# Optimization experiments

Hardware: AMD Instinct MI355X
Metric: run time of the kernel (lower is better)

## Reference

```python
import jax, jax.numpy as jnp
import numpy as np

B = 16384
IN = 512
H = 512

def setup_inputs() -> dict:
    key = jax.random.key(0)
    k1, k2, k3, k4, k5, k6 = jax.random.split(key, 6)
    s_in = 1.0 / np.sqrt(IN + H)
    return {
        "x": jax.random.normal(k1, (B, IN), dtype=jnp.float32),
        "h": jax.random.normal(k2, (B, H), dtype=jnp.float32),
        # lin_in: (IN+H) -> 2H ; stored as [in_features, out_features]
        "W_in": jax.random.uniform(k3, (IN + H, 2 * H), minval=-s_in, maxval=s_in, dtype=jnp.float32),
        "b_in": jax.random.uniform(k4, (2 * H,), minval=-s_in, maxval=s_in, dtype=jnp.float32),
        # lin_out: (IN+H) -> H
        "W_out": jax.random.uniform(k5, (IN + H, H), minval=-s_in, maxval=s_in, dtype=jnp.float32),
        "b_out": jax.random.uniform(k6, (H,), minval=-s_in, maxval=s_in, dtype=jnp.float32),
    }

def reference(x, h, W_in, b_in, W_out, b_out):
    xh = jnp.concatenate([x, h], axis=1)              # [B, IN+H]
    lin = xh @ W_in + b_in                             # [B, 2H]
    learn_pre, forget_pre = jnp.split(lin, 2, axis=1)  # each [B, H]
    learn = jnp.tanh(learn_pre)
    forget_mult = jax.nn.sigmoid(forget_pre)
    h_new = forget_mult * h + (1.0 - forget_mult) * learn
    xh2 = jnp.concatenate([x, h_new], axis=1)          # [B, IN+H]
    out = jnp.tanh(xh2 @ W_out + b_out)                # [B, H]
    return (out, h_new)
```

## Files before the change

### kernel.cpp

```cpp
#include <hip/hip_runtime.h>
#include <cstdint>

typedef unsigned short ushort_t;
typedef __attribute__((ext_vector_type(4))) float f32x4;
typedef __attribute__((ext_vector_type(8))) __bf16 bf16x8;
typedef __attribute__((ext_vector_type(8))) unsigned short ushort8;

#define NB 16384
#define DK 1024

__device__ __forceinline__ unsigned short f2b(float f) {
    unsigned u = __builtin_bit_cast(unsigned, f);
    unsigned r = u + 0x7fffu + ((u >> 16) & 1u);
    return (unsigned short)(r >> 16);
}
__device__ __forceinline__ float b2f(ushort_t b) {
    unsigned u = ((unsigned)b) << 16;
    return __builtin_bit_cast(float, u);
}
__device__ __forceinline__ float fast_sigmoid(float x) {
    return __fdividef(1.0f, 1.0f + __expf(-x));
}
__device__ __forceinline__ float fast_tanh(float x) {
    return __fdividef(2.0f, 1.0f + __expf(-2.0f * x)) - 1.0f;
}

__device__ __forceinline__ void gll16(const void* g, void* lds) {
    __builtin_amdgcn_global_load_lds(
        (__attribute__((address_space(1))) unsigned int*)(uintptr_t)g,
        (__attribute__((address_space(3))) unsigned int*)(unsigned int)(uintptr_t)lds,
        16, 0, 0);
}


__global__ __launch_bounds__(256) void k_f32_to_bf16(const float* __restrict__ s,
                                                     ushort_t* __restrict__ d) {
    size_t g = (size_t)blockIdx.x * 256 + threadIdx.x;
    const float* p = s + g * 8;
    f32x4 f0 = *(const f32x4*)p;
    f32x4 f1 = *(const f32x4*)(p + 4);
    ushort8 o;
#pragma unroll
    for (int j = 0; j < 4; ++j) { o[j] = f2b(f0[j]); o[j + 4] = f2b(f1[j]); }
    *(ushort8*)(d + g * 8) = o;
}

__global__ __launch_bounds__(256) void k_transpose_w(const float* __restrict__ W,
                                                     ushort_t* __restrict__ Wt, int ncols) {
    __shared__ float tile[32][33];
    int n0 = blockIdx.x * 32, k0 = blockIdx.y * 32;
    int tx = threadIdx.x, ty = threadIdx.y;
#pragma unroll
    for (int i = 0; i < 32; i += 8)
        tile[ty + i][tx] = W[(size_t)(k0 + ty + i) * ncols + n0 + tx];
    __syncthreads();
#pragma unroll
    for (int i = 0; i < 32; i += 8)
        Wt[(size_t)(n0 + ty + i) * DK + k0 + tx] = f2b(tile[tx][ty + i]);
}

__global__ __launch_bounds__(256, 2) void k_gemm1(
    const ushort_t* __restrict__ XB, const ushort_t* __restrict__ HB,
    const ushort_t* __restrict__ WT, const float* __restrict__ b_in,
    float* __restrict__ hnew, ushort_t* __restrict__ HN) {
    __shared__ ushort_t As[2][128 * 32];
    __shared__ ushort_t BsL[2][128 * 32];
    __shared__ ushort_t BsF[2][128 * 32];

    const int t = threadIdx.x;
    const int lane = t & 63;
    const int wave = t >> 6;
    const int wm = wave >> 1, wn = wave & 1;
    const int m0 = blockIdx.x * 128;
    const int n0 = blockIdx.y * 128;

    f32x4 accL[4][4] = {};
    f32x4 accF[4][4] = {};

    const int srow = t >> 2;
    const int skel = (t & 3) * 8;
    const size_t arow = (size_t)(m0 + srow) * 512;
    const ushort_t* gBL = WT + (size_t)(n0 + srow) * DK + skel;
    const ushort_t* gBF = WT + (size_t)(n0 + 512 + srow) * DK + skel;

    auto stage = [&](int it, int buf) {
        const int kt = it * 32;
        const ushort_t* abase =
            (kt < 512) ? (XB + arow + kt + skel) : (HB + arow + (kt - 512) + skel);
        ushort_t* a = &As[buf][t * 8];
        ushort_t* bl = &BsL[buf][t * 8];
        ushort_t* bf = &BsF[buf][t * 8];
        gll16(abase, a);
        gll16(abase + 64 * 512, a + 64 * 32);
        gll16(gBL + kt, bl);
        gll16(gBL + kt + 64 * DK, bl + 64 * 32);
        gll16(gBF + kt, bf);
        gll16(gBF + kt + 64 * DK, bf + 64 * 32);
    };

    const int fr = lane & 15;
    const int kq = (lane >> 4) * 8;

    stage(0, 0);
    int cur = 0;
    for (int it = 0; it < 32; ++it) {
        asm volatile("s_waitcnt vmcnt(0)" ::: "memory");
        __syncthreads();
        if (it + 1 < 32) stage(it + 1, cur ^ 1);

        bf16x8 av[4], blv[4], bfv[4];
#pragma unroll
        for (int i = 0; i < 4; ++i) {
            av[i]  = *(const bf16x8*)(&As[cur][(wm * 64 + i * 16 + fr) * 32 + kq]);
            blv[i] = *(const bf16x8*)(&BsL[cur][(wn * 64 + i * 16 + fr) * 32 + kq]);
            bfv[i] = *(const bf16x8*)(&BsF[cur][(wn * 64 + i * 16 + fr) * 32 + kq]);
        }
#pragma unroll
        for (int i = 0; i < 4; ++i)
#pragma unroll
            for (int j = 0; j < 4; ++j) {
                accL[i][j] = __builtin_amdgcn_mfma_f32_16x16x32_bf16(av[i], blv[j], accL[i][j], 0, 0, 0);
                accF[i][j] = __builtin_amdgcn_mfma_f32_16x16x32_bf16(av[i], bfv[j], accF[i][j], 0, 0, 0);
            }
        cur ^= 1;
    }

    const int fq = lane >> 4;
    float bl4[4], bf4[4];
#pragma unroll
    for (int j = 0; j < 4; ++j) {
        const int c = n0 + wn * 64 + j * 16 + fr;
        bl4[j] = b_in[c];
        bf4[j] = b_in[c + 512];
    }
#pragma unroll
    for (int i = 0; i < 4; ++i)
#pragma unroll
        for (int j = 0; j < 4; ++j) {
            const int c = n0 + wn * 64 + j * 16 + fr;
#pragma unroll
            for (int r = 0; r < 4; ++r) {
                const int row = m0 + wm * 64 + i * 16 + fq * 4 + r;
                float lp = accL[i][j][r] + bl4[j];
                float fp = accF[i][j][r] + bf4[j];
                float hv = b2f(HB[(size_t)row * 512 + c]);
                float fm = fast_sigmoid(fp);
                float lr = fast_tanh(lp);
                float hn = fm * hv + (1.0f - fm) * lr;
                hnew[(size_t)row * 512 + c] = hn;
                HN[(size_t)row * 512 + c] = f2b(hn);
            }
        }
}

__global__ __launch_bounds__(256, 2) void k_gemm2(
    const ushort_t* __restrict__ XB, const ushort_t* __restrict__ HN,
    const ushort_t* __restrict__ WT, const float* __restrict__ b_out,
    float* __restrict__ out) {
    __shared__ ushort_t As[2][128 * 32];
    __shared__ ushort_t Bs[2][128 * 32];

    const int t = threadIdx.x;
    const int lane = t & 63;
    const int wave = t >> 6;
    const int wm = wave >> 1, wn = wave & 1;
    const int m0 = blockIdx.x * 128;
    const int n0 = blockIdx.y * 128;

    f32x4 acc[4][4] = {};

    const int srow = t >> 2;
    const int skel = (t & 3) * 8;
    const size_t arow = (size_t)(m0 + srow) * 512;
    const ushort_t* gB = WT + (size_t)(n0 + srow) * DK + skel;

    auto stage = [&](int it, int buf) {
        const int kt = it * 32;
        const ushort_t* abase =
            (kt < 512) ? (XB + arow + kt + skel) : (HN + arow + (kt - 512) + skel);
        ushort_t* a = &As[buf][t * 8];
        ushort_t* b = &Bs[buf][t * 8];
        gll16(abase, a);
        gll16(abase + 64 * 512, a + 64 * 32);
        gll16(gB + kt, b);
        gll16(gB + kt + 64 * DK, b + 64 * 32);
    };

    const int fr = lane & 15;
    const int kq = (lane >> 4) * 8;

    stage(0, 0);
    int cur = 0;
    for (int it = 0; it < 32; ++it) {
        asm volatile("s_waitcnt vmcnt(0)" ::: "memory");
        __syncthreads();
        if (it + 1 < 32) stage(it + 1, cur ^ 1);

        bf16x8 av[4], bv[4];
#pragma unroll
        for (int i = 0; i < 4; ++i) {
            av[i] = *(const bf16x8*)(&As[cur][(wm * 64 + i * 16 + fr) * 32 + kq]);
            bv[i] = *(const bf16x8*)(&Bs[cur][(wn * 64 + i * 16 + fr) * 32 + kq]);
        }
#pragma unroll
        for (int i = 0; i < 4; ++i)
#pragma unroll
            for (int j = 0; j < 4; ++j)
                acc[i][j] = __builtin_amdgcn_mfma_f32_16x16x32_bf16(av[i], bv[j], acc[i][j], 0, 0, 0);
        cur ^= 1;
    }

    const int fq = lane >> 4;
#pragma unroll
    for (int i = 0; i < 4; ++i)
#pragma unroll
        for (int j = 0; j < 4; ++j) {
            const int c = n0 + wn * 64 + j * 16 + fr;
#pragma unroll
            for (int r = 0; r < 4; ++r) {
                const int row = m0 + wm * 64 + i * 16 + fq * 4 + r;
                out[(size_t)row * 512 + c] = fast_tanh(acc[i][j][r] + b_out[c]);
            }
        }
}

extern "C" void kernel_launch(void* const* d_in, const int* in_sizes, int n_in,
                              void* d_out, int out_size, void* d_ws, size_t ws_size,
                              hipStream_t stream) {
    const float* x = (const float*)d_in[0];
    const float* h = (const float*)d_in[1];
    const float* W_in = (const float*)d_in[2];
    const float* b_in = (const float*)d_in[3];
    const float* W_out = (const float*)d_in[4];
    const float* b_out = (const float*)d_in[5];

    float* out = (float*)d_out;
    float* hnew = out + (size_t)NB * 512;

    ushort_t* XB = (ushort_t*)d_ws;
    ushort_t* HB = XB + (size_t)NB * 512;
    ushort_t* HN = HB + (size_t)NB * 512;
    ushort_t* WTI = HN + (size_t)NB * 512;
    ushort_t* WTO = WTI + (size_t)1024 * 1024;

    k_f32_to_bf16<<<4096, 256, 0, stream>>>(x, XB);
    k_f32_to_bf16<<<4096, 256, 0, stream>>>(h, HB);
    k_transpose_w<<<dim3(32, 32), dim3(32, 8), 0, stream>>>(W_in, WTI, 1024);
    k_transpose_w<<<dim3(16, 32), dim3(32, 8), 0, stream>>>(W_out, WTO, 512);
    k_gemm1<<<dim3(128, 4), 256, 0, stream>>>(XB, HB, WTI, b_in, hnew, HN);
    k_gemm2<<<dim3(128, 4), 256, 0, stream>>>(XB, HN, WTO, b_out, out);
}
```

Before: 93.75 us.

## Triple-buffer LDS staging in both GEMMs with partial vmcnt waits

Both GEMM kernels move from double to triple buffering. Loads for the tile two iterations ahead are issued while the current tile is computed, and the wait is relaxed to a partial vmcnt so one tile's loads stay in flight. MFMA sections are wrapped in s_setprio, and gemm2's launch bounds request 3 blocks per CU. The goal is to hide global load latency; the cost is more LDS per block, which may reduce occupancy for gemm1, along with register pressure from the raised occupancy target in gemm2.

Result: no change. 94.47 us (+0.8%).

```diff
diff --git a/kernel.cpp b/kernel.cpp
--- a/kernel.cpp
+++ b/kernel.cpp
@@ -63,9 +63,9 @@
     const ushort_t* __restrict__ XB, const ushort_t* __restrict__ HB,
     const ushort_t* __restrict__ WT, const float* __restrict__ b_in,
     float* __restrict__ hnew, ushort_t* __restrict__ HN) {
-    __shared__ ushort_t As[2][128 * 32];
-    __shared__ ushort_t BsL[2][128 * 32];
-    __shared__ ushort_t BsF[2][128 * 32];
+    __shared__ ushort_t As[3][128 * 32];
+    __shared__ ushort_t BsL[3][128 * 32];
+    __shared__ ushort_t BsF[3][128 * 32];
 
     const int t = threadIdx.x;
     const int lane = t & 63;
@@ -87,7 +87,7 @@
         const int kt = it * 32;
         const ushort_t* abase =
             (kt < 512) ? (XB + arow + kt + skel) : (HB + arow + (kt - 512) + skel);
-        ushort_t* a = &As[buf][t * 8];
+        ushort_t* a  = &As[buf][t * 8];
         ushort_t* bl = &BsL[buf][t * 8];
         ushort_t* bf = &BsF[buf][t * 8];
         gll16(abase, a);
@@ -102,11 +102,17 @@
     const int kq = (lane >> 4) * 8;
 
     stage(0, 0);
+    stage(1, 1);
     int cur = 0;
     for (int it = 0; it < 32; ++it) {
-        asm volatile("s_waitcnt vmcnt(0)" ::: "memory");
-        __syncthreads();
-        if (it + 1 < 32) stage(it + 1, cur ^ 1);
+        if (it < 31) asm volatile("s_waitcnt vmcnt(6)" ::: "memory");
+        else         asm volatile("s_waitcnt vmcnt(0)" ::: "memory");
+        __builtin_amdgcn_s_barrier();
+        asm volatile("" ::: "memory");
+        __builtin_amdgcn_sched_barrier(0);
+
+        int wbuf = cur - 1; if (wbuf < 0) wbuf = 2;
+        if (it < 30) stage(it + 2, wbuf);
 
         bf16x8 av[4], blv[4], bfv[4];
 #pragma unroll
@@ -115,6 +121,7 @@
             blv[i] = *(const bf16x8*)(&BsL[cur][(wn * 64 + i * 16 + fr) * 32 + kq]);
             bfv[i] = *(const bf16x8*)(&BsF[cur][(wn * 64 + i * 16 + fr) * 32 + kq]);
         }
+        __builtin_amdgcn_s_setprio(1);
 #pragma unroll
         for (int i = 0; i < 4; ++i)
 #pragma unroll
@@ -122,7 +129,8 @@
                 accL[i][j] = __builtin_amdgcn_mfma_f32_16x16x32_bf16(av[i], blv[j], accL[i][j], 0, 0, 0);
                 accF[i][j] = __builtin_amdgcn_mfma_f32_16x16x32_bf16(av[i], bfv[j], accF[i][j], 0, 0, 0);
             }
-        cur ^= 1;
+        __builtin_amdgcn_s_setprio(0);
+        cur = (cur == 2) ? 0 : cur + 1;
     }
 
     const int fq = lane >> 4;
@@ -153,12 +161,12 @@
         }
 }
 
-__global__ __launch_bounds__(256, 2) void k_gemm2(
+__global__ __launch_bounds__(256, 3) void k_gemm2(
     const ushort_t* __restrict__ XB, const ushort_t* __restrict__ HN,
     const ushort_t* __restrict__ WT, const float* __restrict__ b_out,
     float* __restrict__ out) {
-    __shared__ ushort_t As[2][128 * 32];
-    __shared__ ushort_t Bs[2][128 * 32];
+    __shared__ ushort_t As[3][128 * 32];
+    __shared__ ushort_t Bs[3][128 * 32];
 
     const int t = threadIdx.x;
     const int lane = t & 63;
@@ -190,11 +198,17 @@
     const int kq = (lane >> 4) * 8;
 
     stage(0, 0);
+    stage(1, 1);
     int cur = 0;
     for (int it = 0; it < 32; ++it) {
-        asm volatile("s_waitcnt vmcnt(0)" ::: "memory");
-        __syncthreads();
-        if (it + 1 < 32) stage(it + 1, cur ^ 1);
+        if (it < 31) asm volatile("s_waitcnt vmcnt(4)" ::: "memory");
+        else         asm volatile("s_waitcnt vmcnt(0)" ::: "memory");
+        __builtin_amdgcn_s_barrier();
+        asm volatile("" ::: "memory");
+        __builtin_amdgcn_sched_barrier(0);
+
+        int wbuf = cur - 1; if (wbuf < 0) wbuf = 2;
+        if (it < 30) stage(it + 2, wbuf);
 
         bf16x8 av[4], bv[4];
 #pragma unroll
@@ -202,12 +216,14 @@
             av[i] = *(const bf16x8*)(&As[cur][(wm * 64 + i * 16 + fr) * 32 + kq]);
             bv[i] = *(const bf16x8*)(&Bs[cur][(wn * 64 + i * 16 + fr) * 32 + kq]);
         }
+        __builtin_amdgcn_s_setprio(1);
 #pragma unroll
         for (int i = 0; i < 4; ++i)
 #pragma unroll
             for (int j = 0; j < 4; ++j)
                 acc[i][j] = __builtin_amdgcn_mfma_f32_16x16x32_bf16(av[i], bv[j], acc[i][j], 0, 0, 0);
-        cur ^= 1;
+        __builtin_amdgcn_s_setprio(0);
+        cur = (cur == 2) ? 0 : cur + 1;
     }
 
     const int fq = lane >> 4;
```

## Restructure GEMMs into 256-row, 8-wave tiles with XOR-swizzled LDS and interleaved prefetch

Applied to the files above, without the earlier changes.

Both GEMM kernels move to 512-thread blocks with 256x128 output tiles and K-tiles of 64. Global-to-LDS loads are split into quarter-stages issued between MFMA phases, with partial vmcnt waits, raw barriers and s_setprio. The intent is to overlap memory with compute and cut LDS bank conflicts. The bf16 activation and weight buffers are written pre-swizzled (XOR on the column within each 64-element chunk) so LDS reads avoid conflicts, and the two conversion launches are merged into one. The cost is one block per CU, 128KB of LDS in gemm1, and fragile hand-tuned wait counts.

Result: faster. 86.60 us (-7.6%).

```diff
diff --git a/kernel.cpp b/kernel.cpp
--- a/kernel.cpp
+++ b/kernel.cpp
@@ -8,6 +8,8 @@
 
 #define NB 16384
 #define DK 1024
+
+#define MFMA16(a, b, c) __builtin_amdgcn_mfma_f32_16x16x32_bf16(a, b, c, 0, 0, 0)
 
 __device__ __forceinline__ unsigned short f2b(float f) {
     unsigned u = __builtin_bit_cast(unsigned, f);
@@ -33,16 +35,26 @@
 }
 
 
-__global__ __launch_bounds__(256) void k_f32_to_bf16(const float* __restrict__ s,
-                                                     ushort_t* __restrict__ d) {
-    size_t g = (size_t)blockIdx.x * 256 + threadIdx.x;
+__global__ __launch_bounds__(256) void k_cvt(const float* __restrict__ x,
+                                             const float* __restrict__ h,
+                                             ushort_t* __restrict__ XB,
+                                             ushort_t* __restrict__ HB) {
+    int b = blockIdx.x;
+    const float* s;
+    ushort_t* d;
+    if (b < 4096) { s = x; d = XB; } else { s = h; d = HB; b -= 4096; }
+    size_t g = (size_t)b * 256 + threadIdx.x;
     const float* p = s + g * 8;
     f32x4 f0 = *(const f32x4*)p;
     f32x4 f1 = *(const f32x4*)(p + 4);
     ushort8 o;
 #pragma unroll
     for (int j = 0; j < 4; ++j) { o[j] = f2b(f0[j]); o[j + 4] = f2b(f1[j]); }
-    *(ushort8*)(d + g * 8) = o;
+    size_t fi = g * 8;
+    int row = (int)(fi >> 9);
+    int c = (int)(fi & 511);
+    int swc = (c & ~63) | ((c & 63) ^ ((row & 7) << 3));
+    *(ushort8*)(d + (size_t)row * 512 + swc) = o;
 }
 
 __global__ __launch_bounds__(256) void k_transpose_w(const float* __restrict__ W,
@@ -55,171 +67,233 @@
         tile[ty + i][tx] = W[(size_t)(k0 + ty + i) * ncols + n0 + tx];
     __syncthreads();
 #pragma unroll
-    for (int i = 0; i < 32; i += 8)
-        Wt[(size_t)(n0 + ty + i) * DK + k0 + tx] = f2b(tile[tx][ty + i]);
-}
-
-__global__ __launch_bounds__(256, 2) void k_gemm1(
+    for (int i = 0; i < 32; i += 8) {
+        int n = n0 + ty + i;
+        int k = k0 + tx;
+        int kk = (k & ~63) | ((k & 63) ^ ((n & 7) << 3));
+        Wt[(size_t)n * DK + kk] = f2b(tile[tx][ty + i]);
+    }
+}
+
+__global__ __launch_bounds__(512, 1) void k_gemm1(
     const ushort_t* __restrict__ XB, const ushort_t* __restrict__ HB,
     const ushort_t* __restrict__ WT, const float* __restrict__ b_in,
     float* __restrict__ hnew, ushort_t* __restrict__ HN) {
-    __shared__ ushort_t As[2][128 * 32];
-    __shared__ ushort_t BsL[2][128 * 32];
-    __shared__ ushort_t BsF[2][128 * 32];
+    __shared__ ushort_t As[2][2][128 * 64];
+    __shared__ ushort_t Bs[2][2][128 * 64];
 
     const int t = threadIdx.x;
     const int lane = t & 63;
-    const int wave = t >> 6;
-    const int wm = wave >> 1, wn = wave & 1;
-    const int m0 = blockIdx.x * 128;
+    const int wid = t >> 6;
+    const int wm = wid >> 2, wn = wid & 3;
+    const int m0 = blockIdx.x * 256;
     const int n0 = blockIdx.y * 128;
 
-    f32x4 accL[4][4] = {};
-    f32x4 accF[4][4] = {};
-
-    const int srow = t >> 2;
-    const int skel = (t & 3) * 8;
-    const size_t arow = (size_t)(m0 + srow) * 512;
-    const ushort_t* gBL = WT + (size_t)(n0 + srow) * DK + skel;
-    const ushort_t* gBF = WT + (size_t)(n0 + 512 + srow) * DK + skel;
-
-    auto stage = [&](int it, int buf) {
-        const int kt = it * 32;
-        const ushort_t* abase =
-            (kt < 512) ? (XB + arow + kt + skel) : (HB + arow + (kt - 512) + skel);
-        ushort_t* a = &As[buf][t * 8];
-        ushort_t* bl = &BsL[buf][t * 8];
-        ushort_t* bf = &BsF[buf][t * 8];
-        gll16(abase, a);
-        gll16(abase + 64 * 512, a + 64 * 32);
-        gll16(gBL + kt, bl);
-        gll16(gBL + kt + 64 * DK, bl + 64 * 32);
-        gll16(gBF + kt, bf);
-        gll16(gBF + kt + 64 * DK, bf + 64 * 32);
-    };
-
-    const int fr = lane & 15;
-    const int kq = (lane >> 4) * 8;
-
-    stage(0, 0);
-    int cur = 0;
-    for (int it = 0; it < 32; ++it) {
-        asm volatile("s_waitcnt vmcnt(0)" ::: "memory");
-        __syncthreads();
-        if (it + 1 < 32) stage(it + 1, cur ^ 1);
-
-        bf16x8 av[4], blv[4], bfv[4];
-#pragma unroll
-        for (int i = 0; i < 4; ++i) {
-            av[i]  = *(const bf16x8*)(&As[cur][(wm * 64 + i * 16 + fr) * 32 + kq]);
-            blv[i] = *(const bf16x8*)(&BsL[cur][(wn * 64 + i * 16 + fr) * 32 + kq]);
-            bfv[i] = *(const bf16x8*)(&BsF[cur][(wn * 64 + i * 16 + fr) * 32 + kq]);
-        }
-#pragma unroll
-        for (int i = 0; i < 4; ++i)
-#pragma unroll
-            for (int j = 0; j < 4; ++j) {
-                accL[i][j] = __builtin_amdgcn_mfma_f32_16x16x32_bf16(av[i], blv[j], accL[i][j], 0, 0, 0);
-                accF[i][j] = __builtin_amdgcn_mfma_f32_16x16x32_bf16(av[i], bfv[j], accF[i][j], 0, 0, 0);
-            }
-        cur ^= 1;
+    const int srow = t >> 3;
+    const int schk = (t & 7) * 8;
+
+    const int fr = lane & 15, fq = lane >> 4;
+    const int xr = (lane & 7) << 3;
+
+    f32x4 accL[8][2] = {};
+    f32x4 accF[8][2] = {};
+
+#define G1_STAGE_A(tile, half) do { \
+        int kt_ = (tile) * 64; \
+        const ushort_t* s_ = (kt_ < 512) \
+            ? (XB + (size_t)(m0 + (half) * 128 + srow) * 512 + kt_ + schk) \
+            : (HB + (size_t)(m0 + (half) * 128 + srow) * 512 + (kt_ - 512) + schk); \
+        ushort_t* d_ = &As[(tile) & 1][half][t * 8]; \
+        gll16(s_, d_); \
+        gll16(s_ + 64 * 512, d_ + 64 * 64); \
+    } while (0)
+
+#define G1_STAGE_B(tile, half) do { \
+        int kt_ = (tile) * 64; \
+        const ushort_t* s_ = WT + (size_t)((half) * 512 + n0 + srow) * DK + kt_ + schk; \
+        ushort_t* d_ = &Bs[(tile) & 1][half][t * 8]; \
+        gll16(s_, d_); \
+        gll16(s_ + 64 * DK, d_ + 64 * 64); \
+    } while (0)
+
+#define G1_LDA(cb, r, kk) (*(const bf16x8*)&As[cb][wm][((r) * 16 + fr) * 64 + (((kk) * 32 + fq * 8) ^ xr)])
+#define G1_LDB(cb, half, j, kk) (*(const bf16x8*)&Bs[cb][half][(wn * 32 + (j) * 16 + fr) * 64 + (((kk) * 32 + fq * 8) ^ xr)])
+
+    G1_STAGE_A(0, 0); G1_STAGE_A(0, 1); G1_STAGE_B(0, 0); G1_STAGE_B(0, 1);
+    G1_STAGE_A(1, 0);
+
+    bf16x8 a[8], b0, b1;
+    for (int i = 0; i < 16; ++i) {
+        const int cb = i & 1;
+        if (i < 15) G1_STAGE_A(i + 1, 1);
+        if (i < 15) asm volatile("s_waitcnt vmcnt(4)" ::: "memory");
+        else        asm volatile("s_waitcnt vmcnt(0)" ::: "memory");
+        asm volatile("s_barrier" ::: "memory");
+#pragma unroll
+        for (int r = 0; r < 8; ++r) a[r] = G1_LDA(cb, r, 0);
+        b0 = G1_LDB(cb, 0, 0, 0); b1 = G1_LDB(cb, 0, 1, 0);
+        __builtin_amdgcn_s_setprio(1);
+#pragma unroll
+        for (int r = 0; r < 8; ++r) {
+            accL[r][0] = MFMA16(a[r], b0, accL[r][0]);
+            accL[r][1] = MFMA16(a[r], b1, accL[r][1]);
+        }
+        __builtin_amdgcn_s_setprio(0);
+        asm volatile("s_barrier" ::: "memory");
+        if (i < 15) G1_STAGE_B(i + 1, 0);
+        b0 = G1_LDB(cb, 1, 0, 0); b1 = G1_LDB(cb, 1, 1, 0);
+        __builtin_amdgcn_s_setprio(1);
+#pragma unroll
+        for (int r = 0; r < 8; ++r) {
+            accF[r][0] = MFMA16(a[r], b0, accF[r][0]);
+            accF[r][1] = MFMA16(a[r], b1, accF[r][1]);
+        }
+        __builtin_amdgcn_s_setprio(0);
+        asm volatile("s_barrier" ::: "memory");
+        if (i < 15) G1_STAGE_B(i + 1, 1);
+#pragma unroll
+        for (int r = 0; r < 8; ++r) a[r] = G1_LDA(cb, r, 1);
+        b0 = G1_LDB(cb, 0, 0, 1); b1 = G1_LDB(cb, 0, 1, 1);
+        __builtin_amdgcn_s_setprio(1);
+#pragma unroll
+        for (int r = 0; r < 8; ++r) {
+            accL[r][0] = MFMA16(a[r], b0, accL[r][0]);
+            accL[r][1] = MFMA16(a[r], b1, accL[r][1]);
+        }
+        __builtin_amdgcn_s_setprio(0);
+        asm volatile("s_barrier" ::: "memory");
+        if (i < 14) G1_STAGE_A(i + 2, 0);
+        b0 = G1_LDB(cb, 1, 0, 1); b1 = G1_LDB(cb, 1, 1, 1);
+        __builtin_amdgcn_s_setprio(1);
+#pragma unroll
+        for (int r = 0; r < 8; ++r) {
+            accF[r][0] = MFMA16(a[r], b0, accF[r][0]);
+            accF[r][1] = MFMA16(a[r], b1, accF[r][1]);
+        }
+        __builtin_amdgcn_s_setprio(0);
     }
 
-    const int fq = lane >> 4;
-    float bl4[4], bf4[4];
-#pragma unroll
-    for (int j = 0; j < 4; ++j) {
-        const int c = n0 + wn * 64 + j * 16 + fr;
-        bl4[j] = b_in[c];
-        bf4[j] = b_in[c + 512];
+    float blv[2], bfv[2];
+#pragma unroll
+    for (int j = 0; j < 2; ++j) {
+        const int c = n0 + wn * 32 + j * 16 + fr;
+        blv[j] = b_in[c];
+        bfv[j] = b_in[c + 512];
     }
 #pragma unroll
-    for (int i = 0; i < 4; ++i)
-#pragma unroll
-        for (int j = 0; j < 4; ++j) {
-            const int c = n0 + wn * 64 + j * 16 + fr;
-#pragma unroll
-            for (int r = 0; r < 4; ++r) {
-                const int row = m0 + wm * 64 + i * 16 + fq * 4 + r;
-                float lp = accL[i][j][r] + bl4[j];
-                float fp = accF[i][j][r] + bf4[j];
-                float hv = b2f(HB[(size_t)row * 512 + c]);
+    for (int r = 0; r < 8; ++r)
+#pragma unroll
+        for (int j = 0; j < 2; ++j) {
+            const int c = n0 + wn * 32 + j * 16 + fr;
+#pragma unroll
+            for (int rr = 0; rr < 4; ++rr) {
+                const int row = m0 + wm * 128 + r * 16 + fq * 4 + rr;
+                const int swc = (c & ~63) | ((c & 63) ^ ((row & 7) << 3));
+                float lp = accL[r][j][rr] + blv[j];
+                float fp = accF[r][j][rr] + bfv[j];
+                float hv = b2f(HB[(size_t)row * 512 + swc]);
                 float fm = fast_sigmoid(fp);
                 float lr = fast_tanh(lp);
                 float hn = fm * hv + (1.0f - fm) * lr;
                 hnew[(size_t)row * 512 + c] = hn;
-                HN[(size_t)row * 512 + c] = f2b(hn);
+                HN[(size_t)row * 512 + swc] = f2b(hn);
             }
         }
 }
 
-__global__ __launch_bounds__(256, 2) void k_gemm2(
+__global__ __launch_bounds__(512, 1) void k_gemm2(
     const ushort_t* __restrict__ XB, const ushort_t* __restrict__ HN,
     const ushort_t* __restrict__ WT, const float* __restrict__ b_out,
     float* __restrict__ out) {
-    __shared__ ushort_t As[2][128 * 32];
-    __shared__ ushort_t Bs[2][128 * 32];
+    __shared__ ushort_t As[2][2][128 * 64];
+    __shared__ ushort_t Bs[2][128 * 64];
 
     const int t = threadIdx.x;
     const int lane = t & 63;
-    const int wave = t >> 6;
-    const int wm = wave >> 1, wn = wave & 1;
-    const int m0 = blockIdx.x * 128;
+    const int wid = t >> 6;
+    const int wm = wid >> 2, wn = wid & 3;
+    const int m0 = blockIdx.x * 256;
     const int n0 = blockIdx.y * 128;
 
-    f32x4 acc[4][4] = {};
-
-    const int srow = t >> 2;
-    const int skel = (t & 3) * 8;
-    const size_t arow = (size_t)(m0 + srow) * 512;
-    const ushort_t* gB = WT + (size_t)(n0 + srow) * DK + skel;
-
-    auto stage = [&](int it, int buf) {
-        const int kt = it * 32;
-        const ushort_t* abase =
-            (kt < 512) ? (XB + arow + kt + skel) : (HN + arow + (kt - 512) + skel);
-        ushort_t* a = &As[buf][t * 8];
-        ushort_t* b = &Bs[buf][t * 8];
-        gll16(abase, a);
-        gll16(abase + 64 * 512, a + 64 * 32);
-        gll16(gB + kt, b);
-        gll16(gB + kt + 64 * DK, b + 64 * 32);
-    };
-
-    const int fr = lane & 15;
-    const int kq = (lane >> 4) * 8;
-
-    stage(0, 0);
-    int cur = 0;
-    for (int it = 0; it < 32; ++it) {
-        asm volatile("s_waitcnt vmcnt(0)" ::: "memory");
-        __syncthreads();
-        if (it + 1 < 32) stage(it + 1, cur ^ 1);
-
-        bf16x8 av[4], bv[4];
-#pragma unroll
-        for (int i = 0; i < 4; ++i) {
-            av[i] = *(const bf16x8*)(&As[cur][(wm * 64 + i * 16 + fr) * 32 + kq]);
-            bv[i] = *(const bf16x8*)(&Bs[cur][(wn * 64 + i * 16 + fr) * 32 + kq]);
-        }
-#pragma unroll
-        for (int i = 0; i < 4; ++i)
-#pragma unroll
-            for (int j = 0; j < 4; ++j)
-                acc[i][j] = __builtin_amdgcn_mfma_f32_16x16x32_bf16(av[i], bv[j], acc[i][j], 0, 0, 0);
-        cur ^= 1;
+    const int srow = t >> 3;
+    const int schk = (t & 7) * 8;
+    const int fr = lane & 15, fq = lane >> 4;
+    const int xr = (lane & 7) << 3;
+
+    f32x4 acc[8][2] = {};
+
+#define G2_STAGE_A(tile, half) do { \
+        int kt_ = (tile) * 64; \
+        const ushort_t* s_ = (kt_ < 512) \
+            ? (XB + (size_t)(m0 + (half) * 128 + srow) * 512 + kt_ + schk) \
+            : (HN + (size_t)(m0 + (half) * 128 + srow) * 512 + (kt_ - 512) + schk); \
+        ushort_t* d_ = &As[(tile) & 1][half][t * 8]; \
+        gll16(s_, d_); \
+        gll16(s_ + 64 * 512, d_ + 64 * 64); \
+    } while (0)
+
+#define G2_STAGE_Bq(tile, q) do { \
+        int kt_ = (tile) * 64; \
+        const ushort_t* s_ = WT + (size_t)(n0 + (q) * 64 + srow) * DK + kt_ + schk; \
+        ushort_t* d_ = &Bs[(tile) & 1][(q) * 64 * 64 + t * 8]; \
+        gll16(s_, d_); \
+    } while (0)
+
+#define G2_LDA(cb, r, kk) (*(const bf16x8*)&As[cb][wm][((r) * 16 + fr) * 64 + (((kk) * 32 + fq * 8) ^ xr)])
+#define G2_LDB(cb, j, kk) (*(const bf16x8*)&Bs[cb][(wn * 32 + (j) * 16 + fr) * 64 + (((kk) * 32 + fq * 8) ^ xr)])
+
+    G2_STAGE_A(0, 0); G2_STAGE_A(0, 1); G2_STAGE_Bq(0, 0); G2_STAGE_Bq(0, 1);
+    G2_STAGE_A(1, 0);
+
+    bf16x8 a[8], b0, b1;
+    for (int i = 0; i < 16; ++i) {
+        const int cb = i & 1;
+        if (i < 15) G2_STAGE_A(i + 1, 1);
+        if (i < 15) asm volatile("s_waitcnt vmcnt(4)" ::: "memory");
+        else        asm volatile("s_waitcnt vmcnt(0)" ::: "memory");
+        asm volatile("s_barrier" ::: "memory");
+#pragma unroll
+        for (int r = 0; r < 8; ++r) a[r] = G2_LDA(cb, r, 0);
+        b0 = G2_LDB(cb, 0, 0);
+        __builtin_amdgcn_s_setprio(1);
+#pragma unroll
+        for (int r = 0; r < 8; ++r) acc[r][0] = MFMA16(a[r], b0, acc[r][0]);
+        __builtin_amdgcn_s_setprio(0);
+        asm volatile("s_barrier" ::: "memory");
+        if (i < 15) G2_STAGE_Bq(i + 1, 0);
+        b1 = G2_LDB(cb, 1, 0);
+        __builtin_amdgcn_s_setprio(1);
+#pragma unroll
+        for (int r = 0; r < 8; ++r) acc[r][1] = MFMA16(a[r], b1, acc[r][1]);
+        __builtin_amdgcn_s_setprio(0);
+        asm volatile("s_barrier" ::: "memory");
+        if (i < 15) G2_STAGE_Bq(i + 1, 1);
+#pragma unroll
+        for (int r = 0; r < 8; ++r) a[r] = G2_LDA(cb, r, 1);
+        b0 = G2_LDB(cb, 0, 1);
+        __builtin_amdgcn_s_setprio(1);
+#pragma unroll
+        for (int r = 0; r < 8; ++r) acc[r][0] = MFMA16(a[r], b0, acc[r][0]);
+        __builtin_amdgcn_s_setprio(0);
+        asm volatile("s_barrier" ::: "memory");
+        if (i < 14) G2_STAGE_A(i + 2, 0);
+        b1 = G2_LDB(cb, 1, 1);
+        __builtin_amdgcn_s_setprio(1);
+#pragma unroll
+        for (int r = 0; r < 8; ++r) acc[r][1] = MFMA16(a[r], b1, acc[r][1]);
+        __builtin_amdgcn_s_setprio(0);
     }
 
-    const int fq = lane >> 4;
-#pragma unroll
-    for (int i = 0; i < 4; ++i)
-#pragma unroll
-        for (int j = 0; j < 4; ++j) {
-            const int c = n0 + wn * 64 + j * 16 + fr;
-#pragma unroll
-            for (int r = 0; r < 4; ++r) {
-                const int row = m0 + wm * 64 + i * 16 + fq * 4 + r;
-                out[(size_t)row * 512 + c] = fast_tanh(acc[i][j][r] + b_out[c]);
+#pragma unroll
+    for (int r = 0; r < 8; ++r)
+#pragma unroll
+        for (int j = 0; j < 2; ++j) {
+            const int c = n0 + wn * 32 + j * 16 + fr;
+            const float bo = b_out[c];
+#pragma unroll
+            for (int rr = 0; rr < 4; ++rr) {
+                const int row = m0 + wm * 128 + r * 16 + fq * 4 + rr;
+                out[(size_t)row * 512 + c] = fast_tanh(acc[r][j][rr] + bo);
             }
         }
 }
@@ -243,10 +317,9 @@
     ushort_t* WTI = HN + (size_t)NB * 512;
     ushort_t* WTO = WTI + (size_t)1024 * 1024;
 
-    k_f32_to_bf16<<<4096, 256, 0, stream>>>(x, XB);
-    k_f32_to_bf16<<<4096, 256, 0, stream>>>(h, HB);
+    k_cvt<<<8192, 256, 0, stream>>>(x, h, XB, HB);
     k_transpose_w<<<dim3(32, 32), dim3(32, 8), 0, stream>>>(W_in, WTI, 1024);
     k_transpose_w<<<dim3(16, 32), dim3(32, 8), 0, stream>>>(W_out, WTO, 512);
-    k_gemm1<<<dim3(128, 4), 256, 0, stream>>>(XB, HB, WTI, b_in, hnew, HN);
-    k_gemm2<<<dim3(128, 4), 256, 0, stream>>>(XB, HN, WTO, b_out, out);
-}
+    k_gemm1<<<dim3(64, 4), 512, 0, stream>>>(XB, HB, WTI, b_in, hnew, HN);
+    k_gemm2<<<dim3(64, 4), 512, 0, stream>>>(XB, HN, WTO, b_out, out);
+}
```

## Halve gemm1 N-tile to double grid, merge convert and transpose launches

Applied to the files above, without the earlier changes.

Gemm1 now uses 64-column tiles for each of the learn and forget halves instead of 128, so the grid doubles to 1024 blocks and each wave holds fewer accumulators. The aim is better occupancy and load balance across CUs, at the cost of reloading the A tile twice as often. The two bf16 conversion launches are merged into one, as are the two weight transposes, cutting launch overhead.

Result: no change. 93.97 us (+0.2%).

```diff
diff --git a/kernel.cpp b/kernel.cpp
--- a/kernel.cpp
+++ b/kernel.cpp
@@ -8,6 +8,8 @@
 
 #define NB 16384
 #define DK 1024
+
+#define MFMA16(a, b, c) __builtin_amdgcn_mfma_f32_16x16x32_bf16(a, b, c, 0, 0, 0)
 
 __device__ __forceinline__ unsigned short f2b(float f) {
     unsigned u = __builtin_bit_cast(unsigned, f);
@@ -33,9 +35,15 @@
 }
 
 
-__global__ __launch_bounds__(256) void k_f32_to_bf16(const float* __restrict__ s,
-                                                     ushort_t* __restrict__ d) {
-    size_t g = (size_t)blockIdx.x * 256 + threadIdx.x;
+__global__ __launch_bounds__(256) void k_cvt(const float* __restrict__ x,
+                                             const float* __restrict__ h,
+                                             ushort_t* __restrict__ XB,
+                                             ushort_t* __restrict__ HB) {
+    int b = blockIdx.x;
+    const float* s;
+    ushort_t* d;
+    if (b < 4096) { s = x; d = XB; } else { s = h; d = HB; b -= 4096; }
+    size_t g = (size_t)b * 256 + threadIdx.x;
     const float* p = s + g * 8;
     f32x4 f0 = *(const f32x4*)p;
     f32x4 f1 = *(const f32x4*)(p + 4);
@@ -45,11 +53,18 @@
     *(ushort8*)(d + g * 8) = o;
 }
 
-__global__ __launch_bounds__(256) void k_transpose_w(const float* __restrict__ W,
-                                                     ushort_t* __restrict__ Wt, int ncols) {
+__global__ __launch_bounds__(256) void k_transpose_w(const float* __restrict__ Wi,
+                                                     const float* __restrict__ Wo,
+                                                     ushort_t* __restrict__ WTI,
+                                                     ushort_t* __restrict__ WTO) {
+    const int z = blockIdx.z;
+    if (z == 1 && blockIdx.x >= 16) return;
+    const float* W = (z == 0) ? Wi : Wo;
+    ushort_t* Wt = (z == 0) ? WTI : WTO;
+    const int ncols = (z == 0) ? 1024 : 512;
     __shared__ float tile[32][33];
     int n0 = blockIdx.x * 32, k0 = blockIdx.y * 32;
-    int tx = threadIdx.x, ty = threadIdx.y;
+    int tx = threadIdx.x & 31, ty = threadIdx.x >> 5;
 #pragma unroll
     for (int i = 0; i < 32; i += 8)
         tile[ty + i][tx] = W[(size_t)(k0 + ty + i) * ncols + n0 + tx];
@@ -64,18 +79,17 @@
     const ushort_t* __restrict__ WT, const float* __restrict__ b_in,
     float* __restrict__ hnew, ushort_t* __restrict__ HN) {
     __shared__ ushort_t As[2][128 * 32];
-    __shared__ ushort_t BsL[2][128 * 32];
-    __shared__ ushort_t BsF[2][128 * 32];
+    __shared__ ushort_t Bs[2][2][64 * 32];
 
     const int t = threadIdx.x;
     const int lane = t & 63;
     const int wave = t >> 6;
     const int wm = wave >> 1, wn = wave & 1;
     const int m0 = blockIdx.x * 128;
-    const int n0 = blockIdx.y * 128;
-
-    f32x4 accL[4][4] = {};
-    f32x4 accF[4][4] = {};
+    const int n0 = blockIdx.y * 64;
+
+    f32x4 accL[4][2] = {};
+    f32x4 accF[4][2] = {};
 
     const int srow = t >> 2;
     const int skel = (t & 3) * 8;
@@ -88,14 +102,10 @@
         const ushort_t* abase =
             (kt < 512) ? (XB + arow + kt + skel) : (HB + arow + (kt - 512) + skel);
         ushort_t* a = &As[buf][t * 8];
-        ushort_t* bl = &BsL[buf][t * 8];
-        ushort_t* bf = &BsF[buf][t * 8];
         gll16(abase, a);
         gll16(abase + 64 * 512, a + 64 * 32);
-        gll16(gBL + kt, bl);
-        gll16(gBL + kt + 64 * DK, bl + 64 * 32);
-        gll16(gBF + kt, bf);
-        gll16(gBF + kt + 64 * DK, bf + 64 * 32);
+        gll16(gBL + kt, &Bs[buf][0][t * 8]);
+        gll16(gBF + kt, &Bs[buf][1][t * 8]);
     };
 
     const int fr = lane & 15;
@@ -108,41 +118,38 @@
         __syncthreads();
         if (it + 1 < 32) stage(it + 1, cur ^ 1);
 
-        bf16x8 av[4], blv[4], bfv[4];
-#pragma unroll
-        for (int i = 0; i < 4; ++i) {
-            av[i]  = *(const bf16x8*)(&As[cur][(wm * 64 + i * 16 + fr) * 32 + kq]);
-            blv[i] = *(const bf16x8*)(&BsL[cur][(wn * 64 + i * 16 + fr) * 32 + kq]);
-            bfv[i] = *(const bf16x8*)(&BsF[cur][(wn * 64 + i * 16 + fr) * 32 + kq]);
-        }
+        bf16x8 av[4], blv[2], bfv[2];
 #pragma unroll
         for (int i = 0; i < 4; ++i)
-#pragma unroll
-            for (int j = 0; j < 4; ++j) {
-                accL[i][j] = __builtin_amdgcn_mfma_f32_16x16x32_bf16(av[i], blv[j], accL[i][j], 0, 0, 0);
-                accF[i][j] = __builtin_amdgcn_mfma_f32_16x16x32_bf16(av[i], bfv[j], accF[i][j], 0, 0, 0);
+            av[i] = *(const bf16x8*)(&As[cur][(wm * 64 + i * 16 + fr) * 32 + kq]);
+#pragma unroll
+        for (int j = 0; j < 2; ++j) {
+            blv[j] = *(const bf16x8*)(&Bs[cur][0][(wn * 32 + j * 16 + fr) * 32 + kq]);
+            bfv[j] = *(const bf16x8*)(&Bs[cur][1][(wn * 32 + j * 16 + fr) * 32 + kq]);
+        }
+#pragma unroll
+        for (int i = 0; i < 4; ++i)
+#pragma unroll
+            for (int j = 0; j < 2; ++j) {
+                accL[i][j] = MFMA16(av[i], blv[j], accL[i][j]);
+                accF[i][j] = MFMA16(av[i], bfv[j], accF[i][j]);
             }
         cur ^= 1;
     }
 
     const int fq = lane >> 4;
-    float bl4[4], bf4[4];
-#pragma unroll
-    for (int j = 0; j < 4; ++j) {
-        const int c = n0 + wn * 64 + j * 16 + fr;
-        bl4[j] = b_in[c];
-        bf4[j] = b_in[c + 512];
-    }
 #pragma unroll
     for (int i = 0; i < 4; ++i)
 #pragma unroll
-        for (int j = 0; j < 4; ++j) {
-            const int c = n0 + wn * 64 + j * 16 + fr;
-#pragma unroll
-            for (int r = 0; r < 4; ++r) {
-                const int row = m0 + wm * 64 + i * 16 + fq * 4 + r;
-                float lp = accL[i][j][r] + bl4[j];
-                float fp = accF[i][j][r] + bf4[j];
+        for (int j = 0; j < 2; ++j) {
+            const int c = n0 + wn * 32 + j * 16 + fr;
+            const float bl = b_in[c];
+            const float bf = b_in[c + 512];
+#pragma unroll
+            for (int rr = 0; rr < 4; ++rr) {
+                const int row = m0 + wm * 64 + i * 16 + fq * 4 + rr;
+                float lp = accL[i][j][rr] + bl;
+                float fp = accF[i][j][rr] + bf;
                 float hv = b2f(HB[(size_t)row * 512 + c]);
                 float fm = fast_sigmoid(fp);
                 float lr = fast_tanh(lp);
@@ -206,7 +213,7 @@
         for (int i = 0; i < 4; ++i)
 #pragma unroll
             for (int j = 0; j < 4; ++j)
-                acc[i][j] = __builtin_amdgcn_mfma_f32_16x16x32_bf16(av[i], bv[j], acc[i][j], 0, 0, 0);
+                acc[i][j] = MFMA16(av[i], bv[j], acc[i][j]);
         cur ^= 1;
     }
 
@@ -216,10 +223,11 @@
 #pragma unroll
         for (int j = 0; j < 4; ++j) {
             const int c = n0 + wn * 64 + j * 16 + fr;
-#pragma unroll
-            for (int r = 0; r < 4; ++r) {
-                const int row = m0 + wm * 64 + i * 16 + fq * 4 + r;
-                out[(size_t)row * 512 + c] = fast_tanh(acc[i][j][r] + b_out[c]);
+            const float bo = b_out[c];
+#pragma unroll
+            for (int rr = 0; rr < 4; ++rr) {
+                const int row = m0 + wm * 64 + i * 16 + fq * 4 + rr;
+                out[(size_t)row * 512 + c] = fast_tanh(acc[i][j][rr] + bo);
             }
         }
 }
@@ -243,10 +251,8 @@
     ushort_t* WTI = HN + (size_t)NB * 512;
     ushort_t* WTO = WTI + (size_t)1024 * 1024;
 
-    k_f32_to_bf16<<<4096, 256, 0, stream>>>(x, XB);
-    k_f32_to_bf16<<<4096, 256, 0, stream>>>(h, HB);
-    k_transpose_w<<<dim3(32, 32), dim3(32, 8), 0, stream>>>(W_in, WTI, 1024);
-    k_transpose_w<<<dim3(16, 32), dim3(32, 8), 0, stream>>>(W_out, WTO, 512);
-    k_gemm1<<<dim3(128, 4), 256, 0, stream>>>(XB, HB, WTI, b_in, hnew, HN);
+    k_cvt<<<8192, 256, 0, stream>>>(x, h, XB, HB);
+    k_transpose_w<<<dim3(32, 32, 2), 256, 0, stream>>>(W_in, W_out, WTI, WTO);
+    k_gemm1<<<dim3(128, 8), 256, 0, stream>>>(XB, HB, WTI, b_in, hnew, HN);
     k_gemm2<<<dim3(128, 4), 256, 0, stream>>>(XB, HN, WTO, b_out, out);
 }
```
